# Optimization experiments

Measured on AMD Instinct MI355X. Metric: run time of the kernel, lower is better.

Reference implementation:

```python
import jax, jax.numpy as jnp
import numpy as np

EPS = 1.0


def _onedirectional_dist(a, b):
    # a: (B, M), b: (B, N) -> per-batch sum over M of min_n (a_m - b_n)^2
    d2 = (a[:, :, None] - b[:, None, :]) ** 2  # (B, M, N)
    return jnp.min(d2, axis=2).sum(axis=1)  # (B,)


def setup_inputs() -> dict:
    key = jax.random.key(0)
    k1, k2, k3 = jax.random.split(key, 3)
    target = jax.random.uniform(k1, (4, 240, 320), dtype=jnp.float32)
    bin_centers = jax.random.uniform(k2, (4, 256), dtype=jnp.float32)
    mask = jax.random.randint(k3, (4, 240, 320), 0, 2).astype(jnp.bool_)
    return {"target": target, "bin_centers": bin_centers, "mask": mask}


def reference(target, bin_centers, mask):
    # masked path of ChamferDistanceLoss.forward
    max_target = jnp.max(jnp.where(mask, target, -jnp.inf))
    max_center = jnp.max(bin_centers)
    mx = jnp.maximum(max_target, max_center)
    mn = jnp.minimum(max_target, max_center)
    pad_value = mx + (mx - mn) + EPS
    B = bin_centers.shape[0]
    # pad bin_centers with one extra column = pad_value
    mod_centers = jnp.concatenate(
        [bin_centers, jnp.broadcast_to(pad_value, (B, 1)).astype(bin_centers.dtype)],
        axis=1,
    )  # (B, n_bins + 1)
    # invalid target pixels replaced by pad_value
    mod_target = jnp.where(mask, target, pad_value).reshape(B, -1)  # (B, H*W)
    bidir = _onedirectional_dist(mod_centers, mod_target) + _onedirectional_dist(
        mod_target, mod_centers
    )
    return jnp.mean(bidir)
```

## Files before the change

kernel.cpp:

```cpp
#include <hip/hip_runtime.h>
#include <math.h>

#define B 4
#define HW 76800
#define NBINS 256
#define TPB 256
#define D1B 64
#define C1  4
#define D2B 150
#define PXB 512
#define F4T (HW / 4 / TPB)


__global__ __launch_bounds__(256) void kmain(const float* __restrict__ target,
                                             const int* __restrict__ mask,
                                             const float* __restrict__ centers,
                                             float* __restrict__ out) {
    __shared__ __align__(16) float s_c[NBINS];
    __shared__ float s_d1[4][C1];
    __shared__ float s_red[4];
    const int tid = threadIdx.x;
    const int b   = blockIdx.y;
    const int blk = blockIdx.x;
    const float BIG = 1e19f;

    if (blk < D1B) {
        float c[C1], mn[C1];
#pragma unroll
        for (int k = 0; k < C1; ++k) {
            c[k]  = centers[b * NBINS + blk * C1 + k];
            mn[k] = INFINITY;
        }
        const float4* tp = (const float4*)(target + b * HW);
        const int4*   mp = (const int4*)(mask + b * HW);
#pragma unroll 3
        for (int j = 0; j < F4T; ++j) {
            float4 p = tp[j * TPB + tid];
            int4   m = mp[j * TPB + tid];
            float p0 = m.x ? p.x : BIG;
            float p1 = m.y ? p.y : BIG;
            float p2 = m.z ? p.z : BIG;
            float p3 = m.w ? p.w : BIG;
#pragma unroll
            for (int k = 0; k < C1; ++k) {
                float d0 = p0 - c[k], d1 = p1 - c[k];
                float d2 = p2 - c[k], d3 = p3 - c[k];
                mn[k] = fminf(mn[k], fminf(fminf(d0 * d0, d1 * d1),
                                           fminf(d2 * d2, d3 * d3)));
            }
        }
        for (int o = 32; o > 0; o >>= 1) {
#pragma unroll
            for (int k = 0; k < C1; ++k)
                mn[k] = fminf(mn[k], __shfl_down(mn[k], o));
        }
        if ((tid & 63) == 0) {
            int w = tid >> 6;
#pragma unroll
            for (int k = 0; k < C1; ++k) s_d1[w][k] = mn[k];
        }
        __syncthreads();
        if (tid < C1) {
            s_red[tid] = fminf(fminf(s_d1[0][tid], s_d1[1][tid]),
                               fminf(s_d1[2][tid], s_d1[3][tid]));
        }
        __syncthreads();
        if (tid == 0)
            atomicAdd(out, 0.25f * (s_red[0] + s_red[1] + s_red[2] + s_red[3]));
    } else {
        const int blk2 = blk - D1B;
        const int base = b * HW + blk2 * PXB;
        float2 v  = ((const float2*)(target + base))[tid];
        int2   mm = ((const int2*)(mask + base))[tid];
        s_c[tid] = centers[b * NBINS + tid];
        __syncthreads();

        float mn0 = INFINITY, mn1 = INFINITY;
        const float4* s_c4 = (const float4*)s_c;
#pragma unroll 8
        for (int q = 0; q < NBINS / 4; ++q) {
            float4 c = s_c4[q];
            float a0 = v.x - c.x, a1 = v.x - c.y, a2 = v.x - c.z, a3 = v.x - c.w;
            float b0 = v.y - c.x, b1 = v.y - c.y, b2 = v.y - c.z, b3 = v.y - c.w;
            mn0 = fminf(mn0, fminf(fminf(a0 * a0, a1 * a1),
                                   fminf(a2 * a2, a3 * a3)));
            mn1 = fminf(mn1, fminf(fminf(b0 * b0, b1 * b1),
                                   fminf(b2 * b2, b3 * b3)));
        }
        float acc = (mm.x ? mn0 : 0.f) + (mm.y ? mn1 : 0.f);
        for (int o = 32; o > 0; o >>= 1) acc += __shfl_down(acc, o);
        if ((tid & 63) == 0) s_red[tid >> 6] = acc;
        __syncthreads();
        if (tid == 0)
            atomicAdd(out, 0.25f * (s_red[0] + s_red[1] + s_red[2] + s_red[3]));
    }
}

extern "C" void kernel_launch(void* const* d_in, const int* in_sizes, int n_in,
                              void* d_out, int out_size, void* d_ws, size_t ws_size,
                              hipStream_t stream) {
    const float* target  = (const float*)d_in[0];
    const float* centers = (const float*)d_in[1];
    const int*   mask    = (const int*)d_in[2];
    float* out = (float*)d_out;

    dim3 g(D1B + D2B, B);
    kmain<<<g, TPB, 0, stream>>>(target, mask, centers, out);
}
```

Measured before the change: 78.99 us.

## Expand squared distance into FMA form and process four pixels per thread

Rewrites (a-c)^2 as a^2 - 2ac + c^2, so the inner loops do one FMA plus a min per pair instead of a subtract, a multiply and a min. The constant square term is added once after the min. The pixel-side blocks now handle four pixels per thread with half as many blocks, which reuses each shared-memory center load across more pixels. The D1 path also drops one block barrier. The expanded form can lose precision through cancellation, and the masked sentinel is raised to 1e38.

After: 74.99 us (median of 2 runs). 5.1% less time.

```diff
diff --git a/kernel.cpp b/kernel.cpp
--- a/kernel.cpp
+++ b/kernel.cpp
@@ -7,8 +7,8 @@
 #define TPB 256
 #define D1B 64
 #define C1  4
-#define D2B 150
-#define PXB 512
+#define D2B 75
+#define PXB 1024
 #define F4T (HW / 4 / TPB)
 
 
@@ -16,19 +16,21 @@
                                              const int* __restrict__ mask,
                                              const float* __restrict__ centers,
                                              float* __restrict__ out) {
+    __shared__ __align__(16) float s_c2[NBINS];
     __shared__ __align__(16) float s_c[NBINS];
     __shared__ float s_d1[4][C1];
     __shared__ float s_red[4];
     const int tid = threadIdx.x;
     const int b   = blockIdx.y;
     const int blk = blockIdx.x;
-    const float BIG = 1e19f;
+    const float BIG = 1e38f;
 
     if (blk < D1B) {
-        float c[C1], mn[C1];
+        float c[C1], c2[C1], mn[C1];
 #pragma unroll
         for (int k = 0; k < C1; ++k) {
             c[k]  = centers[b * NBINS + blk * C1 + k];
+            c2[k] = c[k] * c[k];
             mn[k] = INFINITY;
         }
         const float4* tp = (const float4*)(target + b * HW);
@@ -37,16 +39,17 @@
         for (int j = 0; j < F4T; ++j) {
             float4 p = tp[j * TPB + tid];
             int4   m = mp[j * TPB + tid];
-            float p0 = m.x ? p.x : BIG;
-            float p1 = m.y ? p.y : BIG;
-            float p2 = m.z ? p.z : BIG;
-            float p3 = m.w ? p.w : BIG;
+            float q0 = p.x + p.x, s0 = m.x ? p.x * p.x : BIG;
+            float q1 = p.y + p.y, s1 = m.y ? p.y * p.y : BIG;
+            float q2 = p.z + p.z, s2 = m.z ? p.z * p.z : BIG;
+            float q3 = p.w + p.w, s3 = m.w ? p.w * p.w : BIG;
 #pragma unroll
             for (int k = 0; k < C1; ++k) {
-                float d0 = p0 - c[k], d1 = p1 - c[k];
-                float d2 = p2 - c[k], d3 = p3 - c[k];
-                mn[k] = fminf(mn[k], fminf(fminf(d0 * d0, d1 * d1),
-                                           fminf(d2 * d2, d3 * d3)));
+                float d0 = fmaf(-c[k], q0, s0);
+                float d1 = fmaf(-c[k], q1, s1);
+                float d2 = fmaf(-c[k], q2, s2);
+                float d3 = fmaf(-c[k], q3, s3);
+                mn[k] = fminf(mn[k], fminf(fminf(d0, d1), fminf(d2, d3)));
             }
         }
         for (int o = 32; o > 0; o >>= 1) {
@@ -60,34 +63,55 @@
             for (int k = 0; k < C1; ++k) s_d1[w][k] = mn[k];
         }
         __syncthreads();
-        if (tid < C1) {
-            s_red[tid] = fminf(fminf(s_d1[0][tid], s_d1[1][tid]),
-                               fminf(s_d1[2][tid], s_d1[3][tid]));
+        if (tid == 0) {
+            float tot = 0.f;
+#pragma unroll
+            for (int k = 0; k < C1; ++k) {
+                float r = fminf(fminf(s_d1[0][k], s_d1[1][k]),
+                                fminf(s_d1[2][k], s_d1[3][k]));
+                tot += r + c2[k];
+            }
+            atomicAdd(out, 0.25f * tot);
         }
-        __syncthreads();
-        if (tid == 0)
-            atomicAdd(out, 0.25f * (s_red[0] + s_red[1] + s_red[2] + s_red[3]));
     } else {
         const int blk2 = blk - D1B;
         const int base = b * HW + blk2 * PXB;
-        float2 v  = ((const float2*)(target + base))[tid];
-        int2   mm = ((const int2*)(mask + base))[tid];
-        s_c[tid] = centers[b * NBINS + tid];
+        float4 v  = ((const float4*)(target + base))[tid];
+        int4   mm = ((const int4*)(mask + base))[tid];
+        {
+            float c = centers[b * NBINS + tid];
+            s_c[tid]  = c;
+            s_c2[tid] = c * c;
+        }
         __syncthreads();
 
+        float q0 = v.x + v.x, q1 = v.y + v.y;
+        float q2 = v.z + v.z, q3 = v.w + v.w;
         float mn0 = INFINITY, mn1 = INFINITY;
-        const float4* s_c4 = (const float4*)s_c;
-#pragma unroll 8
-        for (int q = 0; q < NBINS / 4; ++q) {
-            float4 c = s_c4[q];
-            float a0 = v.x - c.x, a1 = v.x - c.y, a2 = v.x - c.z, a3 = v.x - c.w;
-            float b0 = v.y - c.x, b1 = v.y - c.y, b2 = v.y - c.z, b3 = v.y - c.w;
-            mn0 = fminf(mn0, fminf(fminf(a0 * a0, a1 * a1),
-                                   fminf(a2 * a2, a3 * a3)));
-            mn1 = fminf(mn1, fminf(fminf(b0 * b0, b1 * b1),
-                                   fminf(b2 * b2, b3 * b3)));
+        float mn2 = INFINITY, mn3 = INFINITY;
+        const float4* s_c4  = (const float4*)s_c;
+        const float4* s_c24 = (const float4*)s_c2;
+#pragma unroll 4
+        for (int g = 0; g < NBINS / 4; ++g) {
+            float4 c  = s_c4[g];
+            float4 c2 = s_c24[g];
+            float a0 = fmaf(-c.x, q0, c2.x), a1 = fmaf(-c.y, q0, c2.y);
+            float a2 = fmaf(-c.z, q0, c2.z), a3 = fmaf(-c.w, q0, c2.w);
+            mn0 = fminf(mn0, fminf(fminf(a0, a1), fminf(a2, a3)));
+            float b0 = fmaf(-c.x, q1, c2.x), b1 = fmaf(-c.y, q1, c2.y);
+            float b2 = fmaf(-c.z, q1, c2.z), b3 = fmaf(-c.w, q1, c2.w);
+            mn1 = fminf(mn1, fminf(fminf(b0, b1), fminf(b2, b3)));
+            float e0 = fmaf(-c.x, q2, c2.x), e1 = fmaf(-c.y, q2, c2.y);
+            float e2 = fmaf(-c.z, q2, c2.z), e3 = fmaf(-c.w, q2, c2.w);
+            mn2 = fminf(mn2, fminf(fminf(e0, e1), fminf(e2, e3)));
+            float f0 = fmaf(-c.x, q3, c2.x), f1 = fmaf(-c.y, q3, c2.y);
+            float f2 = fmaf(-c.z, q3, c2.z), f3 = fmaf(-c.w, q3, c2.w);
+            mn3 = fminf(mn3, fminf(fminf(f0, f1), fminf(f2, f3)));
         }
-        float acc = (mm.x ? mn0 : 0.f) + (mm.y ? mn1 : 0.f);
+        float acc = (mm.x ? fmaf(v.x, v.x, mn0) : 0.f)
+                  + (mm.y ? fmaf(v.y, v.y, mn1) : 0.f)
+                  + (mm.z ? fmaf(v.z, v.z, mn2) : 0.f)
+                  + (mm.w ? fmaf(v.w, v.w, mn3) : 0.f);
         for (int o = 32; o > 0; o >>= 1) acc += __shfl_down(acc, o);
         if ((tid & 63) == 0) s_red[tid >> 6] = acc;
         __syncthreads();
```
